# Performance work log

Measured on AMD Instinct MI355X. Metric: run time of the kernel, lower is better.

Reference implementation:

```python
import jax, jax.numpy as jnp
import numpy as np

B, N, D, H = 2, 2048, 1024, 16
DH = D // H            # 64
PH = 3 * DH            # 192 per-head proj dim (module quirk: 3*Dh per head)
P = H * PH             # 3072 total projection width


def setup_inputs() -> dict:
    key = jax.random.key(0)
    ks = jax.random.split(key, 8)
    s = 0.02
    return {
        "input": jax.random.normal(ks[0], (B, N, D), dtype=jnp.float32),
        "q_w": jax.random.normal(ks[1], (D, P), dtype=jnp.float32) * s,
        "q_b": jnp.zeros((P,), dtype=jnp.float32),
        "k_w": jax.random.normal(ks[2], (D, P), dtype=jnp.float32) * s,
        "k_b": jnp.zeros((P,), dtype=jnp.float32),
        "v_w": jax.random.normal(ks[3], (D, P), dtype=jnp.float32) * s,
        "v_b": jnp.zeros((P,), dtype=jnp.float32),
        "o_w": jax.random.normal(ks[4], (P, D), dtype=jnp.float32) * s,
        "o_b": jnp.zeros((D,), dtype=jnp.float32),
    }


def reference(input, q_w, q_b, k_w, k_b, v_w, v_b, o_w, o_b):
    def heads(y):  # [B,N,H*PH] -> [B,H,N,PH]
        return y.reshape(B, N, H, PH).transpose(0, 2, 1, 3)

    q_mat = heads(input @ q_w + q_b)
    # faithful to source: v_mat uses the 'k' projection, k_mat uses the 'v' projection
    v_mat = heads(input @ k_w + k_b)
    k_mat = heads(input @ v_w + v_b)

    scale = 1.0 / jnp.sqrt(jnp.float32(DH * H))  # sqrt(dim), per source
    scores = jnp.einsum('bhnd,bhmd->bhnm', q_mat, k_mat) * scale
    weights = jax.nn.softmax(scores, axis=-1)
    inter = jnp.einsum('bhnm,bhmd->bhnd', weights, v_mat)
    inter = inter.transpose(0, 2, 1, 3).reshape(B, N, P)  # b n (h d)
    return inter @ o_w + o_b
```

## Files before the change

kernel.cpp:

```cpp
#include <hip/hip_runtime.h>
#include <cstdint>
#include <cstddef>

typedef __bf16 bf16;
typedef __attribute__((ext_vector_type(8))) __bf16 bf16x8;
typedef __attribute__((ext_vector_type(4))) __bf16 bf16x4;
typedef __attribute__((ext_vector_type(2))) __bf16 bf16x2;
typedef __attribute__((ext_vector_type(4))) float f32x4;

#define MFMA_16x16x32(a, b, c) __builtin_amdgcn_mfma_f32_16x16x32_bf16((a), (b), (c), 0, 0, 0)

#define VMCNT(N) asm volatile("s_waitcnt vmcnt(" #N ")" ::: "memory")
#define LGK0                                           \
  {                                                    \
    asm volatile("s_waitcnt lgkmcnt(0)" ::: "memory"); \
    __builtin_amdgcn_sched_barrier(0);                 \
  }

__device__ __forceinline__ void gload_lds16(const void* g, void* l) {
  __builtin_amdgcn_global_load_lds((__attribute__((address_space(1))) void*)g,
                                   (__attribute__((address_space(3))) void*)l,
                                   16, 0, 0);
}

__device__ __forceinline__ uint32_t pack2(float a, float b) {
  bf16x2 h = {(bf16)a, (bf16)b};
  return __builtin_bit_cast(uint32_t, h);
}

__global__ __launch_bounds__(256) void prep_kernel(const float* __restrict__ X,
                                                   const float* __restrict__ q_w,
                                                   const float* __restrict__ v_w,
                                                   const float* __restrict__ k_w,
                                                   const float* __restrict__ o_w,
                                                   bf16* __restrict__ Xb,
                                                   bf16* __restrict__ Wqkv,
                                                   bf16* __restrict__ Wot) {
  __shared__ float tile[32][33];
  int blk = blockIdx.x;
  if (blk < 4096) {
    int i = blk * 256 + threadIdx.x;
    float4 v = ((const float4*)X)[i];
    bf16x4 o = {(bf16)v.x, (bf16)v.y, (bf16)v.z, (bf16)v.w};
    ((bf16x4*)Xb)[i] = o;
    return;
  }
  const float* in;
  bf16* out;
  int R, C, t;
  if (blk < 13312) {
    t = blk - 4096;
    int widx = t / 3072;
    t -= widx * 3072;
    in = widx == 0 ? q_w : (widx == 1 ? v_w : k_w);
    out = Wqkv + (size_t)widx * 3072 * 1024;
    R = 1024;
    C = 3072;
  } else {
    t = blk - 13312;
    in = o_w;
    out = Wot;
    R = 3072;
    C = 1024;
  }
  int tiles_c = C >> 5;
  int br = t / tiles_c, bc = t % tiles_c;
  int r0 = br << 5, c0 = bc << 5;
  int tr = threadIdx.x >> 5, tc = threadIdx.x & 31;
#pragma unroll
  for (int i = 0; i < 4; i++)
    tile[tr + 8 * i][tc] = in[(size_t)(r0 + tr + 8 * i) * C + c0 + tc];
  __syncthreads();
#pragma unroll
  for (int i = 0; i < 4; i++) {
    int oc = tr + 8 * i;
    out[(size_t)(c0 + oc) * R + r0 + tc] = (bf16)tile[tc][oc];
  }
}

__global__ __launch_bounds__(512, 2) void gemm_fused_qkv(
    const bf16* __restrict__ A, const bf16* __restrict__ Bt,
    const float* __restrict__ q_b, const float* __restrict__ v_b,
    const float* __restrict__ k_b,
    bf16* __restrict__ Qm, bf16* __restrict__ Km, bf16* __restrict__ Vt) {
  constexpr int K = 1024, NT = 16;
  __shared__ __align__(16) bf16 sA[2][2][128 * 32];
  __shared__ __align__(16) bf16 sB[2][192 * 64];

  int bid = blockIdx.x;
  int xcd = bid & 7, j = bid >> 3;
  int bm = xcd * 4 + (j & 3), bn = j >> 2;
  int m0 = bm << 7, n0 = bn * 192;

  int tid = threadIdx.x, lane = tid & 63, w = tid >> 6;
  int wr = w >> 2, wc = w & 3;
  int l15 = lane & 15, lg = lane >> 4;

  int sra = lane >> 2, sca = lane & 3;
  const bf16* gA = A + (size_t)(m0 + w * 16 + sra) * K + ((sca ^ ((sra >> 1) & 3)) * 8);
  int srb = lane >> 3, scb = lane & 7;
  const bf16* gB = Bt + (size_t)(n0 + w * 24 + srb) * K + ((scb ^ srb) * 8);

#define STAGE_AB(BUF, T)                                                   \
  {                                                                        \
    _Pragma("unroll") for (int kh = 0; kh < 2; kh++)                       \
        gload_lds16(gA + (size_t)(T) * 64 + kh * 32, &sA[BUF][kh][w * 512]); \
    _Pragma("unroll") for (int ii = 0; ii < 3; ii++)                       \
        gload_lds16(gB + (size_t)(ii * 8) * K + (T) * 64,                  \
                    &sB[BUF][(w * 3 + ii) * 512]);                         \
  }

  int slotA = lg ^ ((l15 >> 1) & 3);
  int aBase = wr * 2048 + l15 * 32 + slotA * 8;
  int bBase = (wc * 48 + l15) * 64;
  int sB0 = (lg ^ (l15 & 7)) * 8;
  int sB1 = ((4 + lg) ^ (l15 & 7)) * 8;

#define RD_A(BUF, KH)                                                      \
  _Pragma("unroll") for (int mf = 0; mf < 4; mf++)                         \
      a[mf] = *(const bf16x8*)&sA[BUF][KH][aBase + mf * 512];
#define RD_B(BUF, SLOT)                                                    \
  _Pragma("unroll") for (int nf = 0; nf < 3; nf++)                         \
      b[nf] = *(const bf16x8*)&sB[BUF][bBase + nf * 1024 + (SLOT)];
#define MFMA12                                                             \
  _Pragma("unroll") for (int mf = 0; mf < 4; mf++)                         \
      _Pragma("unroll") for (int nf = 0; nf < 3; nf++)                     \
          acc[mf][nf] = MFMA_16x16x32(a[mf], b[nf], acc[mf][nf]);

  f32x4 acc[4][3];
#pragma unroll
  for (int mf = 0; mf < 4; mf++)
#pragma unroll
    for (int nf = 0; nf < 3; nf++) acc[mf][nf] = (f32x4){0.f, 0.f, 0.f, 0.f};

  STAGE_AB(0, 0);

#pragma unroll 2
  for (int s = 0; s < NT; s++) {
    int buf = s & 1, nbuf = buf ^ 1;
    int nxt = (s + 1) & (NT - 1);
    bf16x8 a[4], b[3];

    STAGE_AB(nbuf, nxt);
    VMCNT(5);
    __builtin_amdgcn_s_barrier();

    RD_A(buf, 0);
    RD_B(buf, sB0);
    LGK0;
    __builtin_amdgcn_s_setprio(1);
    MFMA12;
    __builtin_amdgcn_s_setprio(0);

    RD_A(buf, 1);
    RD_B(buf, sB1);
    LGK0;
    __builtin_amdgcn_s_barrier();
    __builtin_amdgcn_s_setprio(1);
    MFMA12;
    __builtin_amdgcn_s_setprio(0);
  }

  const float scl2 = 0.03125f * 1.44269504f;
  int seg = bn >> 4;
  int segbn = bn & 15;
  const float* bias = seg == 0 ? q_b : (seg == 1 ? v_b : k_b);
  bf16* outQK = seg == 0 ? Qm : Km;
#pragma unroll
  for (int mf = 0; mf < 4; mf++) {
#pragma unroll
    for (int nf = 0; nf < 3; nf++) {
      int colL = segbn * 192 + wc * 48 + nf * 16 + l15;
      int row0 = m0 + wr * 64 + mf * 16 + lg * 4;
      float bv = bias[colL];
      if (seg == 0) {
#pragma unroll
        for (int r = 0; r < 4; r++)
          outQK[(size_t)(row0 + r) * 3072 + colL] = (bf16)((acc[mf][nf][r] + bv) * scl2);
      } else if (seg == 1) {
#pragma unroll
        for (int r = 0; r < 4; r++)
          outQK[(size_t)(row0 + r) * 3072 + colL] = (bf16)(acc[mf][nf][r] + bv);
      } else {
        int hh = colL / 192, dd = colL % 192;
        int bi = row0 >> 11, nn = row0 & 2047;
        int jj = (nn >> 2) & 7;
        int nnp = (nn & ~31) | ((jj & 3) << 3) | ((jj >> 2) << 2);
        bf16x4 pk = {(bf16)(acc[mf][nf][0] + bv), (bf16)(acc[mf][nf][1] + bv),
                     (bf16)(acc[mf][nf][2] + bv), (bf16)(acc[mf][nf][3] + bv)};
        *(bf16x4*)(Vt + (((size_t)bi * 16 + hh) * 192 + dd) * 2048 + nnp) = pk;
      }
    }
  }
#undef STAGE_AB
#undef RD_A
#undef RD_B
#undef MFMA12
}

__global__ __launch_bounds__(256, 3) void gemm_oproj(const bf16* __restrict__ A,
                                                     const bf16* __restrict__ Bt,
                                                     const float* __restrict__ bias,
                                                     float* __restrict__ out) {
  constexpr int K = 3072, NT = 48;
  __shared__ __align__(16) bf16 sA[2][2][128 * 32];
  __shared__ __align__(16) bf16 sB[2][2][64 * 32];

  int bid = blockIdx.x;
  int xcd = bid & 7, j = bid >> 3;
  int bm = xcd * 4 + (j & 3), bn = j >> 2;
  int m0 = bm << 7, n0 = bn << 6;

  int tid = threadIdx.x, lane = tid & 63, w = tid >> 6;
  int wr = w >> 1, wc = w & 1;
  int l15 = lane & 15, lg = lane >> 4;

  int sra = lane >> 2, sca = lane & 3;
  int swzS = (sca ^ ((sra >> 1) & 3)) * 8;
  const bf16* gA = A + (size_t)(m0 + w * 32 + sra) * K + swzS;
  const bf16* gB = Bt + (size_t)(n0 + w * 16 + sra) * K + swzS;

#define O_STAGE(BUF, T)                                                     \
  {                                                                         \
    _Pragma("unroll") for (int kh = 0; kh < 2; kh++) {                      \
      _Pragma("unroll") for (int ii = 0; ii < 2; ii++)                      \
          gload_lds16(gA + (size_t)(ii * 16) * K + (T) * 64 + kh * 32,      \
                      &sA[BUF][kh][(w * 32 + ii * 16) * 32]);               \
      gload_lds16(gB + (size_t)(T) * 64 + kh * 32, &sB[BUF][kh][w * 512]);  \
    }                                                                       \
  }

  int slotA = lg ^ ((l15 >> 1) & 3);
  int aBase = (wr * 64 + l15) * 32 + slotA * 8;
  int bBase = (wc * 32 + l15) * 32 + slotA * 8;

#define O_RD(BUF, KH)                                                      \
  {                                                                        \
    _Pragma("unroll") for (int mf = 0; mf < 4; mf++)                       \
        a[mf] = *(const bf16x8*)&sA[BUF][KH][aBase + mf * 512];             \
    _Pragma("unroll") for (int nf = 0; nf < 2; nf++)                       \
        b[nf] = *(const bf16x8*)&sB[BUF][KH][bBase + nf * 512];             \
  }
#define O_MFMA8                                                            \
  _Pragma("unroll") for (int mf = 0; mf < 4; mf++)                         \
      _Pragma("unroll") for (int nf = 0; nf < 2; nf++)                     \
          acc[mf][nf] = MFMA_16x16x32(a[mf], b[nf], acc[mf][nf]);

  f32x4 acc[4][2];
#pragma unroll
  for (int mf = 0; mf < 4; mf++)
#pragma unroll
    for (int nf = 0; nf < 2; nf++) acc[mf][nf] = (f32x4){0.f, 0.f, 0.f, 0.f};

  O_STAGE(0, 0);

#pragma unroll 2
  for (int s = 0; s < NT; s++) {
    int buf = s & 1, nbuf = buf ^ 1;
    int nxt = s + 1 < NT ? s + 1 : 0;
    bf16x8 a[4], b[2];

    O_STAGE(nbuf, nxt);
    VMCNT(6);
    __builtin_amdgcn_s_barrier();

    O_RD(buf, 0);
    LGK0;
    __builtin_amdgcn_s_setprio(1);
    O_MFMA8;
    __builtin_amdgcn_s_setprio(0);

    O_RD(buf, 1);
    LGK0;
    __builtin_amdgcn_s_barrier();
    __builtin_amdgcn_s_setprio(1);
    O_MFMA8;
    __builtin_amdgcn_s_setprio(0);
  }

#pragma unroll
  for (int mf = 0; mf < 4; mf++) {
#pragma unroll
    for (int nf = 0; nf < 2; nf++) {
      int col = n0 + wc * 32 + nf * 16 + l15;
      int row0 = m0 + wr * 64 + mf * 16 + lg * 4;
      float bv = bias[col];
#pragma unroll
      for (int r = 0; r < 4; r++)
        out[(size_t)(row0 + r) * 1024 + col] = acc[mf][nf][r] + bv;
    }
  }
#undef O_STAGE
#undef O_RD
#undef O_MFMA8
}

__global__ __launch_bounds__(512, 2) void attn_kernel(const bf16* __restrict__ Q,
                                                      const bf16* __restrict__ Km,
                                                      const bf16* __restrict__ Vt,
                                                      bf16* __restrict__ inter) {
  __shared__ __align__(16) bf16 sK[2][32 * 192];
  __shared__ __align__(16) bf16 sV[2][192 * 32];

  int i = blockIdx.x;
  int j = i >> 3;
  int bh = (i & 7) * 4 + (j >> 4);
  int qt = j & 15;
  int b = bh >> 4, h = bh & 15;
  int tid = threadIdx.x, lane = tid & 63, w = tid >> 6;
  int l15 = lane & 15, lg = lane >> 4;
  int swz = l15 & 7;

  const bf16* Qh = Q + (size_t)b * 2048 * 3072 + (size_t)h * 192;
  const bf16* Kh = Km + (size_t)b * 2048 * 3072 + (size_t)h * 192;
  const bf16* Vh = Vt + (size_t)bh * 192 * 2048;

  int q0 = qt * 128 + w * 16;

  const bf16* gsrc[3];
  int gstride[3];
  bf16* lbase[3];
#pragma unroll
  for (int ii = 0; ii < 3; ii++) {
    int g = ii * 512 + tid;
    if (g < 768) {
      int krow = g / 24, kc = g % 24;
      int kcs = (kc & 24) | ((kc & 7) ^ (krow & 7));
      gsrc[ii] = Kh + krow * 3072 + kcs * 8;
      gstride[ii] = 32 * 3072;
      lbase[ii] = &sK[0][g * 8];
    } else {
      int gg = g - 768;
      int vrow = gg >> 2, vc = gg & 3;
      int vcs = vc ^ ((vrow >> 1) & 3);
      gsrc[ii] = Vh + vrow * 2048 + vcs * 8;
      gstride[ii] = 32;
      lbase[ii] = &sV[0][gg * 8];
    }
  }

#define STAGE(BUF, KT)                                                      \
  {                                                                         \
    _Pragma("unroll") for (int ii = 0; ii < 3; ii++)                        \
        gload_lds16(gsrc[ii] + (size_t)(KT) * gstride[ii],                  \
                    lbase[ii] + (BUF) * 6144);                              \
  }

  STAGE(0, 0);

  bf16x8 aq[6];
#pragma unroll
  for (int kc = 0; kc < 6; kc++)
    aq[kc] = *(const bf16x8*)(Qh + (size_t)(q0 + l15) * 3072 + kc * 32 + lg * 8);

  f32x4 o[12];
#pragma unroll
  for (int df = 0; df < 12; df++) o[df] = (f32x4){0.f, 0.f, 0.f, 0.f};
  float lsum = 0.f;

  int cv = lg ^ ((l15 >> 1) & 3);

  __syncthreads();

  for (int kt = 0; kt < 64; kt++) {
    const bf16* kbuf = sK[kt & 1];
    const bf16* vbuf = sV[kt & 1];
    if (kt < 63) STAGE((kt & 1) ^ 1, kt + 1);

    f32x4 st[2];
    st[0] = (f32x4){0.f, 0.f, 0.f, 0.f};
    st[1] = (f32x4){0.f, 0.f, 0.f, 0.f};
    __builtin_amdgcn_s_setprio(1);
#pragma unroll
    for (int kc = 0; kc < 6; kc++) {
      int g = kc * 4 + lg;
      int cc = (g & 24) | ((g & 7) ^ swz);
#pragma unroll
      for (int kf = 0; kf < 2; kf++) {
        bf16x8 bk = *(const bf16x8*)&kbuf[(kf * 16 + l15) * 192 + cc * 8];
        st[kf] = MFMA_16x16x32(bk, aq[kc], st[kf]);
      }
    }
    __builtin_amdgcn_s_setprio(0);

    float e00 = exp2f(st[0][0]), e01 = exp2f(st[0][1]);
    float e02 = exp2f(st[0][2]), e03 = exp2f(st[0][3]);
    float e10 = exp2f(st[1][0]), e11 = exp2f(st[1][1]);
    float e12 = exp2f(st[1][2]), e13 = exp2f(st[1][3]);
    lsum += ((e00 + e01) + (e02 + e03)) + ((e10 + e11) + (e12 + e13));
    union { uint32_t u[4]; bf16x8 v; } fb;
    fb.u[0] = pack2(e00, e01);
    fb.u[1] = pack2(e02, e03);
    fb.u[2] = pack2(e10, e11);
    fb.u[3] = pack2(e12, e13);
    bf16x8 pf = fb.v;

    __builtin_amdgcn_s_setprio(1);
#pragma unroll
    for (int df = 0; df < 12; df++) {
      bf16x8 av = *(const bf16x8*)&vbuf[(df * 16 + l15) * 32 + cv * 8];
      o[df] = MFMA_16x16x32(av, pf, o[df]);
    }
    __builtin_amdgcn_s_setprio(0);

    __syncthreads();
  }

  {
    lsum += __shfl_xor(lsum, 16);
    lsum += __shfl_xor(lsum, 32);
    float inv = 1.0f / lsum;
    size_t token = (size_t)b * 2048 + q0 + l15;
    bf16* outp = inter + token * 3072 + h * 192 + lg * 4;
#pragma unroll
    for (int df = 0; df < 12; df++) {
      bf16x4 pk = {(bf16)(o[df][0] * inv), (bf16)(o[df][1] * inv),
                   (bf16)(o[df][2] * inv), (bf16)(o[df][3] * inv)};
      *(bf16x4*)(outp + df * 16) = pk;
    }
  }
#undef STAGE
}

extern "C" void kernel_launch(void* const* d_in, const int* in_sizes, int n_in,
                              void* d_out, int out_size, void* d_ws, size_t ws_size,
                              hipStream_t stream) {
  const float* X = (const float*)d_in[0];
  const float* q_w = (const float*)d_in[1];
  const float* q_b = (const float*)d_in[2];
  const float* k_w = (const float*)d_in[3];
  const float* k_b = (const float*)d_in[4];
  const float* v_w = (const float*)d_in[5];
  const float* v_b = (const float*)d_in[6];
  const float* o_w = (const float*)d_in[7];
  const float* o_b = (const float*)d_in[8];

  char* ws = (char*)d_ws;
  bf16* Xb  = (bf16*)(ws);
  bf16* Wqt = (bf16*)(ws + 8388608);
  bf16* Wot = (bf16*)(ws + 27262976);
  bf16* Qm  = (bf16*)(ws + 33554432);
  bf16* Km  = (bf16*)(ws + 58720256);
  bf16* Vtw = (bf16*)(ws + 83886080);
  bf16* Im  = (bf16*)(ws + 109051904);

  prep_kernel<<<16384, 256, 0, stream>>>(X, q_w, v_w, k_w, o_w, Xb, Wqt, Wot);

  gemm_fused_qkv<<<1536, 512, 0, stream>>>(Xb, Wqt, q_b, v_b, k_b, Qm, Km, Vtw);

  attn_kernel<<<512, 512, 0, stream>>>(Qm, Km, Vtw, Im);

  gemm_oproj<<<512, 256, 0, stream>>>(Im, Wot, o_b, (float*)d_out);
}
```

Before: 254.7 us.

## Double attention query rows per wave to reuse K/V LDS fragments

Each wave now processes two 16-row query fragments (256 query rows per block), so every K and V fragment read from LDS feeds two MFMAs instead of one. This halves the grid to 256 blocks and halves the total K/V global traffic. Register use grows because accumulators and Q fragments double, so launch bounds drop to one block per SM. The cost is lower occupancy and only 256 blocks across the CUs, which may leave some compute units idle.

```diff
diff --git a/kernel.cpp b/kernel.cpp
--- a/kernel.cpp
+++ b/kernel.cpp
@@ -295,7 +295,7 @@
 #undef O_MFMA8
 }
 
-__global__ __launch_bounds__(512, 2) void attn_kernel(const bf16* __restrict__ Q,
+__global__ __launch_bounds__(512, 1) void attn_kernel(const bf16* __restrict__ Q,
                                                       const bf16* __restrict__ Km,
                                                       const bf16* __restrict__ Vt,
                                                       bf16* __restrict__ inter) {
@@ -304,8 +304,8 @@
 
   int i = blockIdx.x;
   int j = i >> 3;
-  int bh = (i & 7) * 4 + (j >> 4);
-  int qt = j & 15;
+  int bh = (i & 7) * 4 + (j >> 3);
+  int qt = j & 7;
   int b = bh >> 4, h = bh & 15;
   int tid = threadIdx.x, lane = tid & 63, w = tid >> 6;
   int l15 = lane & 15, lg = lane >> 4;
@@ -315,7 +315,7 @@
   const bf16* Kh = Km + (size_t)b * 2048 * 3072 + (size_t)h * 192;
   const bf16* Vh = Vt + (size_t)bh * 192 * 2048;
 
-  int q0 = qt * 128 + w * 16;
+  int q0 = qt * 256 + w * 32;
 
   const bf16* gsrc[3];
   int gstride[3];
@@ -348,15 +348,19 @@
 
   STAGE(0, 0);
 
-  bf16x8 aq[6];
-#pragma unroll
-  for (int kc = 0; kc < 6; kc++)
-    aq[kc] = *(const bf16x8*)(Qh + (size_t)(q0 + l15) * 3072 + kc * 32 + lg * 8);
-
-  f32x4 o[12];
-#pragma unroll
-  for (int df = 0; df < 12; df++) o[df] = (f32x4){0.f, 0.f, 0.f, 0.f};
-  float lsum = 0.f;
+  bf16x8 aq[2][6];
+#pragma unroll
+  for (int rf = 0; rf < 2; rf++)
+#pragma unroll
+    for (int kc = 0; kc < 6; kc++)
+      aq[rf][kc] = *(const bf16x8*)(Qh + (size_t)(q0 + rf * 16 + l15) * 3072 + kc * 32 + lg * 8);
+
+  f32x4 o[2][12];
+#pragma unroll
+  for (int rf = 0; rf < 2; rf++)
+#pragma unroll
+    for (int df = 0; df < 12; df++) o[rf][df] = (f32x4){0.f, 0.f, 0.f, 0.f};
+  float lsum[2] = {0.f, 0.f};
 
   int cv = lg ^ ((l15 >> 1) & 3);
 
@@ -367,9 +371,11 @@
     const bf16* vbuf = sV[kt & 1];
     if (kt < 63) STAGE((kt & 1) ^ 1, kt + 1);
 
-    f32x4 st[2];
-    st[0] = (f32x4){0.f, 0.f, 0.f, 0.f};
-    st[1] = (f32x4){0.f, 0.f, 0.f, 0.f};
+    f32x4 st[2][2];
+#pragma unroll
+    for (int kf = 0; kf < 2; kf++)
+#pragma unroll
+      for (int rf = 0; rf < 2; rf++) st[kf][rf] = (f32x4){0.f, 0.f, 0.f, 0.f};
     __builtin_amdgcn_s_setprio(1);
 #pragma unroll
     for (int kc = 0; kc < 6; kc++) {
@@ -378,44 +384,52 @@
 #pragma unroll
       for (int kf = 0; kf < 2; kf++) {
         bf16x8 bk = *(const bf16x8*)&kbuf[(kf * 16 + l15) * 192 + cc * 8];
-        st[kf] = MFMA_16x16x32(bk, aq[kc], st[kf]);
+        st[kf][0] = MFMA_16x16x32(bk, aq[0][kc], st[kf][0]);
+        st[kf][1] = MFMA_16x16x32(bk, aq[1][kc], st[kf][1]);
       }
     }
     __builtin_amdgcn_s_setprio(0);
 
-    float e00 = exp2f(st[0][0]), e01 = exp2f(st[0][1]);
-    float e02 = exp2f(st[0][2]), e03 = exp2f(st[0][3]);
-    float e10 = exp2f(st[1][0]), e11 = exp2f(st[1][1]);
-    float e12 = exp2f(st[1][2]), e13 = exp2f(st[1][3]);
-    lsum += ((e00 + e01) + (e02 + e03)) + ((e10 + e11) + (e12 + e13));
-    union { uint32_t u[4]; bf16x8 v; } fb;
-    fb.u[0] = pack2(e00, e01);
-    fb.u[1] = pack2(e02, e03);
-    fb.u[2] = pack2(e10, e11);
-    fb.u[3] = pack2(e12, e13);
-    bf16x8 pf = fb.v;
+    bf16x8 pf[2];
+#pragma unroll
+    for (int rf = 0; rf < 2; rf++) {
+      float e00 = exp2f(st[0][rf][0]), e01 = exp2f(st[0][rf][1]);
+      float e02 = exp2f(st[0][rf][2]), e03 = exp2f(st[0][rf][3]);
+      float e10 = exp2f(st[1][rf][0]), e11 = exp2f(st[1][rf][1]);
+      float e12 = exp2f(st[1][rf][2]), e13 = exp2f(st[1][rf][3]);
+      lsum[rf] += ((e00 + e01) + (e02 + e03)) + ((e10 + e11) + (e12 + e13));
+      union { uint32_t u[4]; bf16x8 v; } fb;
+      fb.u[0] = pack2(e00, e01);
+      fb.u[1] = pack2(e02, e03);
+      fb.u[2] = pack2(e10, e11);
+      fb.u[3] = pack2(e12, e13);
+      pf[rf] = fb.v;
+    }
 
     __builtin_amdgcn_s_setprio(1);
 #pragma unroll
     for (int df = 0; df < 12; df++) {
       bf16x8 av = *(const bf16x8*)&vbuf[(df * 16 + l15) * 32 + cv * 8];
-      o[df] = MFMA_16x16x32(av, pf, o[df]);
+      o[0][df] = MFMA_16x16x32(av, pf[0], o[0][df]);
+      o[1][df] = MFMA_16x16x32(av, pf[1], o[1][df]);
     }
     __builtin_amdgcn_s_setprio(0);
 
     __syncthreads();
   }
 
-  {
-    lsum += __shfl_xor(lsum, 16);
-    lsum += __shfl_xor(lsum, 32);
-    float inv = 1.0f / lsum;
-    size_t token = (size_t)b * 2048 + q0 + l15;
+#pragma unroll
+  for (int rf = 0; rf < 2; rf++) {
+    float ls = lsum[rf];
+    ls += __shfl_xor(ls, 16);
+    ls += __shfl_xor(ls, 32);
+    float inv = 1.0f / ls;
+    size_t token = (size_t)b * 2048 + q0 + rf * 16 + l15;
     bf16* outp = inter + token * 3072 + h * 192 + lg * 4;
 #pragma unroll
     for (int df = 0; df < 12; df++) {
-      bf16x4 pk = {(bf16)(o[df][0] * inv), (bf16)(o[df][1] * inv),
-                   (bf16)(o[df][2] * inv), (bf16)(o[df][3] * inv)};
+      bf16x4 pk = {(bf16)(o[rf][df][0] * inv), (bf16)(o[rf][df][1] * inv),
+                   (bf16)(o[rf][df][2] * inv), (bf16)(o[rf][df][3] * inv)};
       *(bf16x4*)(outp + df * 16) = pk;
     }
   }
@@ -448,7 +462,7 @@
 
   gemm_fused_qkv<<<1536, 512, 0, stream>>>(Xb, Wqt, q_b, v_b, k_b, Qm, Km, Vtw);
 
-  attn_kernel<<<512, 512, 0, stream>>>(Qm, Km, Vtw, Im);
+  attn_kernel<<<256, 512, 0, stream>>>(Qm, Km, Vtw, Im);
 
   gemm_oproj<<<512, 256, 0, stream>>>(Im, Wot, o_b, (float*)d_out);
 }
```

Result: faster. 249.1 us (median of 2 runs) (-2.2%).
